# Kernel tuning notes

Hardware: AMD Instinct MI355X
Metric: run time of the kernel (lower is better)

## Reference

```python
import jax, jax.numpy as jnp
import numpy as np

B, S, DIM = 2, 4096, 768
G = DIM // 3          # gate_dim = 256
H, DK = 4, G // 4     # heads=4, d_k=64
SCALE = 1.0 / np.sqrt(DK)


def setup_inputs() -> dict:
    key = jax.random.key(0)
    ks = jax.random.split(key, 9)
    r = lambda k, shp, s: (jax.random.normal(k, shp, dtype=jnp.float32) * s)
    w_s = 1.0 / np.sqrt(G)
    return {
        "x": r(ks[0], (B, S, DIM), 1.0),
        "wq": r(ks[1], (G, G), w_s), "bq": r(ks[2], (G,), 0.01),
        "wk": r(ks[3], (G, G), w_s), "bk": r(ks[4], (G,), 0.01),
        "wv": r(ks[5], (G, G), w_s), "bv": r(ks[6], (G,), 0.01),
        "wo": r(ks[7], (G, G), w_s), "bo": r(ks[8], (G,), 0.01),
    }


def reference(x, wq, bq, wk, bk, wv, bv, wo, bo):
    # chunk(3, dim=-1): q/k/v slices of width G
    xq, xk, xv = x[..., :G], x[..., G:2 * G], x[..., 2 * G:3 * G]
    # linear projections then split into heads: [b, s, h, d]
    q = (xq @ wq.T + bq).reshape(B, S, H, DK)
    k = (xk @ wk.T + bk).reshape(B, S, H, DK)
    v = (xv @ wv.T + bv).reshape(B, S, H, DK)
    scores = jnp.einsum('bihd,bjhd->bijh', q, k) * SCALE  # [b, i, j, h]
    # NOTE: original applies Softmax(dim=1) -> over the QUERY axis i
    attn = jax.nn.softmax(scores, axis=1)
    out = jnp.einsum('bijh,bjhd->bihd', attn, v).reshape(B, S, G)
    return out @ wo.T + bo
```

## Files before the change

### kernel.cpp

```cpp
#include <hip/hip_runtime.h>

#define SEQ   4096
#define HH    4
#define SCALE 0.125f
#define SC2   0.18033688011112042f
#define C16   -23.083120654223414f

typedef __bf16 bf16x8 __attribute__((ext_vector_type(8)));
typedef __bf16 bf16x4 __attribute__((ext_vector_type(4)));
typedef float  f32x4  __attribute__((ext_vector_type(4)));

constexpr size_t OFF_W16  = 0;
constexpr size_t OFF_A    = 131072;
constexpr size_t OFF_AO   = 294912;
constexpr size_t OFF_X16  = 9732096;
constexpr size_t OFF_Q16  = 12877824;
constexpr size_t K16OFF   = 2097152;
constexpr size_t V16OFF   = 4194304;
constexpr size_t OFF_PZ   = 16023552;

__device__ __forceinline__ f32x4 mf(bf16x8 a, bf16x8 b, f32x4 c) {
    return __builtin_amdgcn_mfma_f32_16x16x32_bf16(a, b, c, 0, 0, 0);
}

__device__ __forceinline__ void gload16(const __bf16* g, __bf16* l) {
    __builtin_amdgcn_global_load_lds(
        (const __attribute__((address_space(1))) unsigned int*)g,
        (__attribute__((address_space(3))) unsigned int*)l, 16, 0, 0);
}

__device__ __forceinline__ float ex2(float x) {
    return __builtin_amdgcn_exp2f(x);
}

__global__ void k_prep(const float* __restrict__ x,
                       const float* __restrict__ wq, const float* __restrict__ wk,
                       const float* __restrict__ wv, const float* __restrict__ wo,
                       float* __restrict__ ws) {
    int bx = blockIdx.x, t = threadIdx.x;
    if (bx < 6144) {
        size_t i4 = ((size_t)bx * 256 + t) * 4;
        float4 v = *(const float4*)(x + i4);
        bf16x4 o = {(__bf16)v.x, (__bf16)v.y, (__bf16)v.z, (__bf16)v.w};
        *(bf16x4*)((__bf16*)(ws + OFF_X16) + i4) = o;
    } else if (bx < 6400) {
        int q = bx - 6144;
        int y = q >> 6;
        const float* src = (y == 0) ? wq : (y == 1) ? wk : (y == 2) ? wv : wo;
        float sc = (y == 0) ? SC2 : 1.0f;
        size_t i4 = ((size_t)(q & 63) * 256 + t) * 4;
        float4 v = *(const float4*)(src + i4);
        bf16x4 o = {(__bf16)(v.x * sc), (__bf16)(v.y * sc),
                    (__bf16)(v.z * sc), (__bf16)(v.w * sc)};
        *(bf16x4*)((__bf16*)(ws + OFF_W16) + (size_t)y * 65536 + i4) = o;
    } else {
        size_t i4 = ((size_t)(bx - 6400) * 256 + t) * 4;
        *(float4*)(ws + OFF_AO + i4) = make_float4(0.f, 0.f, 0.f, 0.f);
    }
}

__global__ __launch_bounds__(256) void k_qkv_mfma(const float* __restrict__ bq,
                                                  const float* __restrict__ bk,
                                                  const float* __restrict__ bv,
                                                  float* __restrict__ ws) {
    int t = threadIdx.x, lane = t & 63, w = t >> 6;
    int yw = blockIdx.y;
    int ntb = blockIdx.z * 8;
    int row0 = blockIdx.x * 64 + w * 16;
    int mrow = lane & 15, quad = lane >> 4;
    const __bf16* X16 = (const __bf16*)(ws + OFF_X16);
    const __bf16* W16 = (const __bf16*)(ws + OFF_W16) + (size_t)yw * 65536;
    const float* bias = (yw == 0) ? bq : (yw == 1) ? bk : bv;
    __bf16* Qb = (__bf16*)(ws + OFF_Q16);
    f32x4 acc[8];
#pragma unroll
    for (int n = 0; n < 8; n++) acc[n] = {0.f, 0.f, 0.f, 0.f};
    const __bf16* ap = X16 + (size_t)(row0 + mrow) * 768 + yw * 256 + quad * 8;
    const __bf16* bp = W16 + (size_t)ntb * 4096 + (size_t)mrow * 256 + quad * 8;
    for (int kc = 0; kc < 256; kc += 32) {
        bf16x8 a = *(const bf16x8*)(ap + kc);
#pragma unroll
        for (int nt = 0; nt < 8; nt++) {
            bf16x8 b = *(const bf16x8*)(bp + (size_t)nt * 4096 + kc);
            acc[nt] = mf(a, b, acc[nt]);
        }
    }
#pragma unroll
    for (int nt = 0; nt < 8; nt++) {
        int n = (ntb + nt) * 16 + mrow;
        float bb = bias[n];
        if (yw == 0) bb *= SC2;
        int h = n >> 6, d = n & 63;
#pragma unroll
        for (int r = 0; r < 4; r++) {
            int sg = row0 + quad * 4 + r;
            int b_ = sg >> 12, s = sg & 4095;
            int bh = b_ * HH + h;
            float val = acc[nt][r] + bb;
            if (yw == 0) {
                int tile = s >> 4, m = s & 15, frag = d >> 5, q2 = (d >> 3) & 3, e = d & 7;
                size_t idx = (((size_t)bh * 256 + tile) * 2 + frag) * 512 +
                             (size_t)(q2 * 16 + m) * 8 + e;
                Qb[idx] = (__bf16)val;
            } else if (yw == 1) {
                int jc = s >> 5, jj = s & 31;
                int tl = (jj >> 2) & 1, m = ((jj >> 3) << 2) | (jj & 3);
                int frag = d >> 5, q2 = (d >> 3) & 3, e = d & 7;
                size_t idx = (((size_t)bh * 128 + jc) * 4 + tl * 2 + frag) * 512 +
                             (size_t)(q2 * 16 + m) * 8 + e;
                Qb[K16OFF + idx] = (__bf16)val;
            } else {
                int jc = s >> 5, qk = (s >> 3) & 3, e = s & 7;
                int nd = d >> 4, nl = d & 15;
                size_t idx = (((size_t)bh * 128 + jc) * 4 + nd) * 512 +
                             (size_t)(qk * 16 + nl) * 8 + e;
                Qb[V16OFF + idx] = (__bf16)val;
            }
        }
    }
}

__global__ __launch_bounds__(256) void k_colstats(float* __restrict__ ws) {
    __shared__ __bf16 qbuf[2][4096];
    int t = threadIdx.x, lane = t & 63, w = t >> 6;
    int jb = blockIdx.x, iy = blockIdx.y, bh = blockIdx.z;
    int jc0 = jb * 8 + w * 2;
    const __bf16* Qp = (const __bf16*)(ws + OFF_Q16);
    const __bf16* Kp = Qp + K16OFF;
    const __bf16* kb = Kp + ((size_t)(bh * 128 + jc0) * 4) * 512 + lane * 8;
    bf16x8 kA0 = *(const bf16x8*)(kb);
    bf16x8 kA1 = *(const bf16x8*)(kb + 512);
    bf16x8 kB0 = *(const bf16x8*)(kb + 1024);
    bf16x8 kB1 = *(const bf16x8*)(kb + 1536);
    bf16x8 kC0 = *(const bf16x8*)(kb + 2048);
    bf16x8 kC1 = *(const bf16x8*)(kb + 2560);
    bf16x8 kD0 = *(const bf16x8*)(kb + 3072);
    bf16x8 kD1 = *(const bf16x8*)(kb + 3584);
    const __bf16* q0 = Qp + ((size_t)(bh * 256 + iy * 16) * 2) * 512 +
                       w * 1024 + lane * 8;
    gload16(q0, qbuf[0] + w * 1024);
    gload16(q0 + 512, qbuf[0] + w * 1024 + 512);
    __syncthreads();
    const f32x4 cin = {C16, C16, C16, C16};
    float z0 = 0.f, z1 = 0.f, z2 = 0.f, z3 = 0.f;
    for (int ic = 0; ic < 4; ic++) {
        const __bf16* cur = qbuf[ic & 1];
        if (ic < 3) {
            const __bf16* qn = Qp + ((size_t)(bh * 256 + iy * 16 + (ic + 1) * 4) * 2) * 512 +
                               w * 1024 + lane * 8;
            gload16(qn, qbuf[(ic + 1) & 1] + w * 1024);
            gload16(qn + 512, qbuf[(ic + 1) & 1] + w * 1024 + 512);
        }
#pragma unroll
        for (int it = 0; it < 4; it++) {
            bf16x8 a0 = *(const bf16x8*)(cur + it * 1024 + lane * 8);
            bf16x8 a1 = *(const bf16x8*)(cur + it * 1024 + 512 + lane * 8);
            f32x4 cA = mf(a0, kA0, cin); cA = mf(a1, kA1, cA);
            f32x4 cB = mf(a0, kB0, cin); cB = mf(a1, kB1, cB);
            f32x4 cC = mf(a0, kC0, cin); cC = mf(a1, kC1, cC);
            f32x4 cD = mf(a0, kD0, cin); cD = mf(a1, kD1, cD);
#pragma unroll
            for (int r = 0; r < 4; r++) {
                z0 += ex2(cA[r]);
                z1 += ex2(cB[r]);
                z2 += ex2(cC[r]);
                z3 += ex2(cD[r]);
            }
        }
        __syncthreads();
    }
    z0 += __shfl_xor(z0, 16, 64);
    z0 += __shfl_xor(z0, 32, 64);
    z1 += __shfl_xor(z1, 16, 64);
    z1 += __shfl_xor(z1, 32, 64);
    z2 += __shfl_xor(z2, 16, 64);
    z2 += __shfl_xor(z2, 32, 64);
    z3 += __shfl_xor(z3, 16, 64);
    z3 += __shfl_xor(z3, 32, 64);
    if (lane < 16) {
        size_t o = OFF_PZ + (size_t)iy * 32768 + (size_t)bh * SEQ +
                   jc0 * 32 + ((lane >> 2) << 3) + (lane & 3);
        ws[o] = z0;
        ws[o + 4] = z1;
        ws[o + 32] = z2;
        ws[o + 36] = z3;
    }
}

__global__ void k_afin(float* __restrict__ ws) {
    int idx = blockIdx.x * 256 + threadIdx.x;
    const float* pz = ws + OFF_PZ;
    float Z = 0.f;
#pragma unroll
    for (int y = 0; y < 16; y++) Z += pz[(size_t)y * 32768 + idx];
    ws[OFF_A + idx] = 1.0f / Z;
}

__global__ void k_vnorm(float* __restrict__ ws) {
    int f = blockIdx.x * 256 + threadIdx.x;
    __bf16* V = (__bf16*)(ws + OFF_Q16) + V16OFF;
    const float* R = ws + OFF_A;
    size_t base = (size_t)f * 8;
    int c = f >> 6;
    int p0 = (int)(base & 511);
    int bh = c >> 9, jc = (c >> 2) & 127;
    int qk = p0 >> 7;
    int jb = jc * 32 + qk * 8;
    const float* r = R + (size_t)bh * SEQ + jb;
    bf16x8 v = *(const bf16x8*)(V + base);
    f32x4 r0 = *(const f32x4*)(r);
    f32x4 r1 = *(const f32x4*)(r + 4);
    bf16x8 o;
#pragma unroll
    for (int e = 0; e < 4; e++) {
        o[e]     = (__bf16)((float)v[e] * r0[e]);
        o[4 + e] = (__bf16)((float)v[4 + e] * r1[e]);
    }
    *(bf16x8*)(V + base) = o;
}

__global__ __launch_bounds__(256) void k_attnpv(float* __restrict__ ws) {
    __shared__ __align__(16) char pool[24576];
    int t = threadIdx.x, lane = t & 63, w = t >> 6;
    int jy = blockIdx.y, bh = blockIdx.z;
    int itp = blockIdx.x * 4 + w;
    int it0 = itp * 2;
    int mrow = lane & 15, quad = lane >> 4;
    const __bf16* Qp = (const __bf16*)(ws + OFF_Q16);
    const __bf16* Kp = Qp + K16OFF;
    const __bf16* Vp = Qp + V16OFF;

    const __bf16* qb = Qp + ((size_t)(bh * 256 + it0) * 2) * 512 + lane * 8;
    bf16x8 aq00 = *(const bf16x8*)(qb);
    bf16x8 aq01 = *(const bf16x8*)(qb + 512);
    bf16x8 aq10 = *(const bf16x8*)(qb + 1024);
    bf16x8 aq11 = *(const bf16x8*)(qb + 1536);

    f32x4 oT0[4], oT1[4];
#pragma unroll
    for (int nd = 0; nd < 4; nd++) {
        oT0[nd] = {0.f, 0.f, 0.f, 0.f};
        oT1[nd] = {0.f, 0.f, 0.f, 0.f};
    }
    const f32x4 cin = {C16, C16, C16, C16};
    int c0g = jy * 32;
    const __bf16* kg = Kp + ((size_t)(bh * 128 + c0g) * 4) * 512 + w * 512 + lane * 8;
    const __bf16* vg = Vp + ((size_t)(bh * 128 + c0g) * 4) * 512 + w * 512 + lane * 8;
    gload16(kg, (__bf16*)pool + w * 512);
    gload16(vg, (__bf16*)(pool + 4096) + w * 512);
    kg += 2048; vg += 2048;
    __syncthreads();

    int bc = 0;
    for (int jt = 0; jt < 32; ++jt) {
        int bn = (bc == 2) ? 0 : bc + 1;
        if (jt < 31) {
            gload16(kg, (__bf16*)(pool + bn * 8192) + w * 512);
            gload16(vg, (__bf16*)(pool + bn * 8192 + 4096) + w * 512);
            kg += 2048; vg += 2048;
            asm volatile("s_waitcnt vmcnt(2)" ::: "memory");
        } else {
            asm volatile("s_waitcnt vmcnt(0)" ::: "memory");
        }
        __builtin_amdgcn_s_barrier();
        const __bf16* curK = (const __bf16*)(pool + bc * 8192);
        const __bf16* curV = (const __bf16*)(pool + bc * 8192 + 4096);
        bf16x8 ck0 = *(const bf16x8*)(curK + lane * 8);
        bf16x8 ck1 = *(const bf16x8*)(curK + 512 + lane * 8);
        bf16x8 ck2 = *(const bf16x8*)(curK + 1024 + lane * 8);
        bf16x8 ck3 = *(const bf16x8*)(curK + 1536 + lane * 8);
        f32x4 c00 = mf(ck0, aq00, cin); c00 = mf(ck1, aq01, c00);
        f32x4 c01 = mf(ck2, aq00, cin); c01 = mf(ck3, aq01, c01);
        f32x4 c10 = mf(ck0, aq10, cin); c10 = mf(ck1, aq11, c10);
        f32x4 c11 = mf(ck2, aq10, cin); c11 = mf(ck3, aq11, c11);
        bf16x8 pb0, pb1;
#pragma unroll
        for (int r = 0; r < 4; r++) {
            pb0[r]     = (__bf16)ex2(c00[r]);
            pb0[4 + r] = (__bf16)ex2(c01[r]);
            pb1[r]     = (__bf16)ex2(c10[r]);
            pb1[4 + r] = (__bf16)ex2(c11[r]);
        }
#pragma unroll
        for (int nd = 0; nd < 4; nd++) {
            bf16x8 bv = *(const bf16x8*)(curV + nd * 512 + lane * 8);
            oT0[nd] = mf(bv, pb0, oT0[nd]);
            oT1[nd] = mf(bv, pb1, oT1[nd]);
        }
        bc = bn;
    }
    __syncthreads();

    float* sO = (float*)pool + (size_t)w * 1040;
    int b = bh >> 2, h = bh & 3;
    float* AO = ws + OFF_AO;
    int i0 = it0 * 16;
#pragma unroll
    for (int nd = 0; nd < 4; nd++)
#pragma unroll
        for (int r = 0; r < 4; r++)
            sO[mrow * 65 + nd * 16 + quad * 4 + r] = oT0[nd][r];
#pragma unroll
    for (int c = 0; c < 16; c++)
        atomicAdd(&AO[((size_t)(b * SEQ + i0 + c)) * 256 + h * 64 + lane],
                  sO[c * 65 + lane]);
#pragma unroll
    for (int nd = 0; nd < 4; nd++)
#pragma unroll
        for (int r = 0; r < 4; r++)
            sO[mrow * 65 + nd * 16 + quad * 4 + r] = oT1[nd][r];
#pragma unroll
    for (int c = 0; c < 16; c++)
        atomicAdd(&AO[((size_t)(b * SEQ + i0 + 16 + c)) * 256 + h * 64 + lane],
                  sO[c * 65 + lane]);
}

__global__ __launch_bounds__(256) void k_outproj_mfma(const float* __restrict__ bo,
                                                      float* __restrict__ ws,
                                                      float* __restrict__ out) {
    int t = threadIdx.x, lane = t & 63, w = t >> 6;
    int row0 = blockIdx.x * 64 + w * 16;
    int ntb = blockIdx.y * 4;
    int mrow = lane & 15, quad = lane >> 4;
    const float* AO = ws + OFF_AO;
    const __bf16* W16 = (const __bf16*)(ws + OFF_W16) + (size_t)3 * 65536;
    f32x4 acc[4];
#pragma unroll
    for (int n = 0; n < 4; n++) acc[n] = {0.f, 0.f, 0.f, 0.f};
    const float* ap = AO + (size_t)(row0 + mrow) * 256 + quad * 8;
    const __bf16* bp = W16 + (size_t)ntb * 4096 + (size_t)mrow * 256 + quad * 8;
    for (int kc = 0; kc < 256; kc += 32) {
        float4 u = *(const float4*)(ap + kc);
        float4 v = *(const float4*)(ap + kc + 4);
        bf16x8 a = {(__bf16)u.x, (__bf16)u.y, (__bf16)u.z, (__bf16)u.w,
                    (__bf16)v.x, (__bf16)v.y, (__bf16)v.z, (__bf16)v.w};
#pragma unroll
        for (int nt = 0; nt < 4; nt++) {
            bf16x8 b = *(const bf16x8*)(bp + (size_t)nt * 4096 + kc);
            acc[nt] = mf(a, b, acc[nt]);
        }
    }
#pragma unroll
    for (int nt = 0; nt < 4; nt++) {
        int n = (ntb + nt) * 16 + mrow;
        float bb = bo[n];
#pragma unroll
        for (int r = 0; r < 4; r++) {
            int sg = row0 + quad * 4 + r;
            out[(size_t)sg * 256 + n] = acc[nt][r] + bb;
        }
    }
}

extern "C" void kernel_launch(void* const* d_in, const int* in_sizes, int n_in,
                              void* d_out, int out_size, void* d_ws, size_t ws_size,
                              hipStream_t stream) {
    const float* x  = (const float*)d_in[0];
    const float* wq = (const float*)d_in[1];
    const float* bq = (const float*)d_in[2];
    const float* wk = (const float*)d_in[3];
    const float* bk = (const float*)d_in[4];
    const float* wv = (const float*)d_in[5];
    const float* bv = (const float*)d_in[6];
    const float* wo = (const float*)d_in[7];
    const float* bo = (const float*)d_in[8];
    float* ws = (float*)d_ws;
    float* out = (float*)d_out;

    k_prep<<<8448, 256, 0, stream>>>(x, wq, wk, wv, wo, ws);
    k_qkv_mfma<<<dim3(128, 3, 2), 256, 0, stream>>>(bq, bk, bv, ws);
    k_colstats<<<dim3(16, 16, 8), 256, 0, stream>>>(ws);
    k_afin<<<128, 256, 0, stream>>>(ws);
    k_vnorm<<<1024, 256, 0, stream>>>(ws);
    k_attnpv<<<dim3(32, 4, 8), 256, 0, stream>>>(ws);
    k_outproj_mfma<<<dim3(128, 4), 256, 0, stream>>>(bo, ws, out);
}
```

Measured before the change: 207.7 us.

## Load Q/K/V straight into registers, dropping LDS staging and barriers

In k_colstats and k_attnpv, the LDS double/triple-buffered async global-to-LDS loads and block barriers are replaced by direct per-wave global loads into registers. In the attention kernel, the next K/V tiles are prefetched into registers, interleaved between the two halves of the MFMA/exp work. Launch bounds now request 4 blocks per CU. The aim is to cut LDS traffic and barrier stalls and raise occupancy. In exchange, every wave in a block now loads the same K/V data redundantly from global/L2 instead of sharing it through LDS.

```diff
diff --git a/kernel.cpp b/kernel.cpp
--- a/kernel.cpp
+++ b/kernel.cpp
@@ -21,12 +21,6 @@
 
 __device__ __forceinline__ f32x4 mf(bf16x8 a, bf16x8 b, f32x4 c) {
     return __builtin_amdgcn_mfma_f32_16x16x32_bf16(a, b, c, 0, 0, 0);
-}
-
-__device__ __forceinline__ void gload16(const __bf16* g, __bf16* l) {
-    __builtin_amdgcn_global_load_lds(
-        (const __attribute__((address_space(1))) unsigned int*)g,
-        (__attribute__((address_space(3))) unsigned int*)l, 16, 0, 0);
 }
 
 __device__ __forceinline__ float ex2(float x) {
@@ -120,8 +114,7 @@
     }
 }
 
-__global__ __launch_bounds__(256) void k_colstats(float* __restrict__ ws) {
-    __shared__ __bf16 qbuf[2][4096];
+__global__ __launch_bounds__(256, 4) void k_colstats(float* __restrict__ ws) {
     int t = threadIdx.x, lane = t & 63, w = t >> 6;
     int jb = blockIdx.x, iy = blockIdx.y, bh = blockIdx.z;
     int jc0 = jb * 8 + w * 2;
@@ -136,38 +129,24 @@
     bf16x8 kC1 = *(const bf16x8*)(kb + 2560);
     bf16x8 kD0 = *(const bf16x8*)(kb + 3072);
     bf16x8 kD1 = *(const bf16x8*)(kb + 3584);
-    const __bf16* q0 = Qp + ((size_t)(bh * 256 + iy * 16) * 2) * 512 +
-                       w * 1024 + lane * 8;
-    gload16(q0, qbuf[0] + w * 1024);
-    gload16(q0 + 512, qbuf[0] + w * 1024 + 512);
-    __syncthreads();
+    const __bf16* qg = Qp + ((size_t)(bh * 256 + iy * 16) * 2) * 512 + lane * 8;
     const f32x4 cin = {C16, C16, C16, C16};
     float z0 = 0.f, z1 = 0.f, z2 = 0.f, z3 = 0.f;
-    for (int ic = 0; ic < 4; ic++) {
-        const __bf16* cur = qbuf[ic & 1];
-        if (ic < 3) {
-            const __bf16* qn = Qp + ((size_t)(bh * 256 + iy * 16 + (ic + 1) * 4) * 2) * 512 +
-                               w * 1024 + lane * 8;
-            gload16(qn, qbuf[(ic + 1) & 1] + w * 1024);
-            gload16(qn + 512, qbuf[(ic + 1) & 1] + w * 1024 + 512);
-        }
-#pragma unroll
-        for (int it = 0; it < 4; it++) {
-            bf16x8 a0 = *(const bf16x8*)(cur + it * 1024 + lane * 8);
-            bf16x8 a1 = *(const bf16x8*)(cur + it * 1024 + 512 + lane * 8);
-            f32x4 cA = mf(a0, kA0, cin); cA = mf(a1, kA1, cA);
-            f32x4 cB = mf(a0, kB0, cin); cB = mf(a1, kB1, cB);
-            f32x4 cC = mf(a0, kC0, cin); cC = mf(a1, kC1, cC);
-            f32x4 cD = mf(a0, kD0, cin); cD = mf(a1, kD1, cD);
-#pragma unroll
-            for (int r = 0; r < 4; r++) {
-                z0 += ex2(cA[r]);
-                z1 += ex2(cB[r]);
-                z2 += ex2(cC[r]);
-                z3 += ex2(cD[r]);
-            }
-        }
-        __syncthreads();
+    for (int tt = 0; tt < 16; tt++) {
+        bf16x8 a0 = *(const bf16x8*)(qg);
+        bf16x8 a1 = *(const bf16x8*)(qg + 512);
+        qg += 1024;
+        f32x4 cA = mf(a0, kA0, cin); cA = mf(a1, kA1, cA);
+        f32x4 cB = mf(a0, kB0, cin); cB = mf(a1, kB1, cB);
+        f32x4 cC = mf(a0, kC0, cin); cC = mf(a1, kC1, cC);
+        f32x4 cD = mf(a0, kD0, cin); cD = mf(a1, kD1, cD);
+#pragma unroll
+        for (int r = 0; r < 4; r++) {
+            z0 += ex2(cA[r]);
+            z1 += ex2(cB[r]);
+            z2 += ex2(cC[r]);
+            z3 += ex2(cD[r]);
+        }
     }
     z0 += __shfl_xor(z0, 16, 64);
     z0 += __shfl_xor(z0, 32, 64);
@@ -219,8 +198,8 @@
     *(bf16x8*)(V + base) = o;
 }
 
-__global__ __launch_bounds__(256) void k_attnpv(float* __restrict__ ws) {
-    __shared__ __align__(16) char pool[24576];
+__global__ __launch_bounds__(256, 4) void k_attnpv(float* __restrict__ ws) {
+    __shared__ float sO[4][1040];
     int t = threadIdx.x, lane = t & 63, w = t >> 6;
     int jy = blockIdx.y, bh = blockIdx.z;
     int itp = blockIdx.x * 4 + w;
@@ -244,54 +223,60 @@
     }
     const f32x4 cin = {C16, C16, C16, C16};
     int c0g = jy * 32;
-    const __bf16* kg = Kp + ((size_t)(bh * 128 + c0g) * 4) * 512 + w * 512 + lane * 8;
-    const __bf16* vg = Vp + ((size_t)(bh * 128 + c0g) * 4) * 512 + w * 512 + lane * 8;
-    gload16(kg, (__bf16*)pool + w * 512);
-    gload16(vg, (__bf16*)(pool + 4096) + w * 512);
+    const __bf16* kg = Kp + ((size_t)(bh * 128 + c0g) * 4) * 512 + lane * 8;
+    const __bf16* vg = Vp + ((size_t)(bh * 128 + c0g) * 4) * 512 + lane * 8;
+    bf16x8 k0 = *(const bf16x8*)(kg);
+    bf16x8 k1 = *(const bf16x8*)(kg + 512);
+    bf16x8 k2 = *(const bf16x8*)(kg + 1024);
+    bf16x8 k3 = *(const bf16x8*)(kg + 1536);
+    bf16x8 v0 = *(const bf16x8*)(vg);
+    bf16x8 v1 = *(const bf16x8*)(vg + 512);
+    bf16x8 v2 = *(const bf16x8*)(vg + 1024);
+    bf16x8 v3 = *(const bf16x8*)(vg + 1536);
     kg += 2048; vg += 2048;
-    __syncthreads();
-
-    int bc = 0;
+
     for (int jt = 0; jt < 32; ++jt) {
-        int bn = (bc == 2) ? 0 : bc + 1;
-        if (jt < 31) {
-            gload16(kg, (__bf16*)(pool + bn * 8192) + w * 512);
-            gload16(vg, (__bf16*)(pool + bn * 8192 + 4096) + w * 512);
-            kg += 2048; vg += 2048;
-            asm volatile("s_waitcnt vmcnt(2)" ::: "memory");
-        } else {
-            asm volatile("s_waitcnt vmcnt(0)" ::: "memory");
-        }
-        __builtin_amdgcn_s_barrier();
-        const __bf16* curK = (const __bf16*)(pool + bc * 8192);
-        const __bf16* curV = (const __bf16*)(pool + bc * 8192 + 4096);
-        bf16x8 ck0 = *(const bf16x8*)(curK + lane * 8);
-        bf16x8 ck1 = *(const bf16x8*)(curK + 512 + lane * 8);
-        bf16x8 ck2 = *(const bf16x8*)(curK + 1024 + lane * 8);
-        bf16x8 ck3 = *(const bf16x8*)(curK + 1536 + lane * 8);
-        f32x4 c00 = mf(ck0, aq00, cin); c00 = mf(ck1, aq01, c00);
-        f32x4 c01 = mf(ck2, aq00, cin); c01 = mf(ck3, aq01, c01);
-        f32x4 c10 = mf(ck0, aq10, cin); c10 = mf(ck1, aq11, c10);
-        f32x4 c11 = mf(ck2, aq10, cin); c11 = mf(ck3, aq11, c11);
-        bf16x8 pb0, pb1;
+        f32x4 c00 = mf(k0, aq00, cin); c00 = mf(k1, aq01, c00);
+        f32x4 c01 = mf(k2, aq00, cin); c01 = mf(k3, aq01, c01);
+        bf16x8 pb0;
 #pragma unroll
         for (int r = 0; r < 4; r++) {
             pb0[r]     = (__bf16)ex2(c00[r]);
             pb0[4 + r] = (__bf16)ex2(c01[r]);
+        }
+        oT0[0] = mf(v0, pb0, oT0[0]);
+        oT0[1] = mf(v1, pb0, oT0[1]);
+        oT0[2] = mf(v2, pb0, oT0[2]);
+        oT0[3] = mf(v3, pb0, oT0[3]);
+        f32x4 c10 = mf(k0, aq10, cin); c10 = mf(k1, aq11, c10);
+        f32x4 c11 = mf(k2, aq10, cin); c11 = mf(k3, aq11, c11);
+        if (jt < 31) {
+            k0 = *(const bf16x8*)(kg);
+            k1 = *(const bf16x8*)(kg + 512);
+            k2 = *(const bf16x8*)(kg + 1024);
+            k3 = *(const bf16x8*)(kg + 1536);
+            kg += 2048;
+        }
+        bf16x8 pb1;
+#pragma unroll
+        for (int r = 0; r < 4; r++) {
             pb1[r]     = (__bf16)ex2(c10[r]);
             pb1[4 + r] = (__bf16)ex2(c11[r]);
         }
-#pragma unroll
-        for (int nd = 0; nd < 4; nd++) {
-            bf16x8 bv = *(const bf16x8*)(curV + nd * 512 + lane * 8);
-            oT0[nd] = mf(bv, pb0, oT0[nd]);
-            oT1[nd] = mf(bv, pb1, oT1[nd]);
-        }
-        bc = bn;
-    }
-    __syncthreads();
-
-    float* sO = (float*)pool + (size_t)w * 1040;
+        oT1[0] = mf(v0, pb1, oT1[0]);
+        oT1[1] = mf(v1, pb1, oT1[1]);
+        oT1[2] = mf(v2, pb1, oT1[2]);
+        oT1[3] = mf(v3, pb1, oT1[3]);
+        if (jt < 31) {
+            v0 = *(const bf16x8*)(vg);
+            v1 = *(const bf16x8*)(vg + 512);
+            v2 = *(const bf16x8*)(vg + 1024);
+            v3 = *(const bf16x8*)(vg + 1536);
+            vg += 2048;
+        }
+    }
+
+    float* so = sO[w];
     int b = bh >> 2, h = bh & 3;
     float* AO = ws + OFF_AO;
     int i0 = it0 * 16;
@@ -299,20 +284,20 @@
     for (int nd = 0; nd < 4; nd++)
 #pragma unroll
         for (int r = 0; r < 4; r++)
-            sO[mrow * 65 + nd * 16 + quad * 4 + r] = oT0[nd][r];
+            so[mrow * 65 + nd * 16 + quad * 4 + r] = oT0[nd][r];
 #pragma unroll
     for (int c = 0; c < 16; c++)
         atomicAdd(&AO[((size_t)(b * SEQ + i0 + c)) * 256 + h * 64 + lane],
-                  sO[c * 65 + lane]);
+                  so[c * 65 + lane]);
 #pragma unroll
     for (int nd = 0; nd < 4; nd++)
 #pragma unroll
         for (int r = 0; r < 4; r++)
-            sO[mrow * 65 + nd * 16 + quad * 4 + r] = oT1[nd][r];
+            so[mrow * 65 + nd * 16 + quad * 4 + r] = oT1[nd][r];
 #pragma unroll
     for (int c = 0; c < 16; c++)
         atomicAdd(&AO[((size_t)(b * SEQ + i0 + 16 + c)) * 256 + h * 64 + lane],
-                  sO[c * 65 + lane]);
+                  so[c * 65 + lane]);
 }
 
 __global__ __launch_bounds__(256) void k_outproj_mfma(const float* __restrict__ bo,
```

Measured after the change: 238.9 us. 1.15x slower.
